# Performance work log

Measured on AMD Instinct MI355X. Metric: run time of the kernel, lower is better.

The kernel has to match this reference:

```python
import jax, jax.numpy as jnp
import numpy as np

EPS = 1e-8
TEMP = 0.1

def setup_inputs() -> dict:
    key = jax.random.key(0)
    k1, k2, k3, k4, k5 = jax.random.split(key, 5)
    B, C, S, D = 4096, 1000, 5, 2048
    return {
        "query": jax.random.normal(k1, (B, D), dtype=jnp.float32),
        "labels": jax.random.randint(k2, (B,), 0, C),
        "memory_keys": jax.random.normal(k3, (C, S, D), dtype=jnp.float32),
        "memory_values": jax.random.normal(k4, (C, S, D), dtype=jnp.float32),
        "quality_scores": jax.random.uniform(k5, (C, S), dtype=jnp.float32),
        "top_k": 3,
    }

def reference(query, labels, memory_keys, memory_values, quality_scores, top_k):
    # Gather per-sample class slices: (B, S, D) and (B, S)
    class_keys = memory_keys[labels]
    class_vals = memory_values[labels]
    class_scores = quality_scores[labels]

    # Cosine similarity between query[i] and its class's slot keys
    qn = query / jnp.maximum(jnp.linalg.norm(query, axis=-1, keepdims=True), EPS)
    kn = class_keys / jnp.maximum(jnp.linalg.norm(class_keys, axis=-1, keepdims=True), EPS)
    sim = jnp.einsum('bd,bsd->bs', qn, kn)           # (B, S)
    combined = sim * class_scores                    # (B, S)

    k = min(int(top_k), class_scores.shape[1])
    top_scores, top_idx = jax.lax.top_k(combined, k) # (B, k)
    attn = jax.nn.softmax(top_scores / TEMP, axis=-1)
    top_vals = jnp.take_along_axis(class_vals, top_idx[..., None], axis=1)  # (B, k, D)
    retrieved = jnp.einsum('bk,bkd->bd', attn, top_vals)                    # (B, D)

    # miss handling: classes whose quality scores sum to 0 yield zeros
    hit = class_scores.sum(axis=1) != 0              # (B,)
    retrieved = jnp.where(hit[:, None], retrieved, 0.0)
    weights = jnp.where(hit, top_scores.mean(axis=-1), 0.0)
    return retrieved, weights
```

## Files before the change

### kernel.cpp

```cpp
#include <hip/hip_runtime.h>
#include <math.h>

#define NSLOT 5
#define EPSF 1e-8f
#define WPB 4

typedef float f4 __attribute__((ext_vector_type(4)));


__global__ void hist_kernel(const int* __restrict__ labels, int* __restrict__ counts, int B) {
    int i = blockIdx.x * blockDim.x + threadIdx.x;
    if (i < B) atomicAdd(&counts[labels[i]], 1);
}

__global__ void scan_kernel(const int* __restrict__ counts, int* __restrict__ cursor, int C) {
    __shared__ int sh[1024];
    __shared__ int running;
    if (threadIdx.x == 0) running = 0;
    __syncthreads();
    for (int base = 0; base < C; base += 1024) {
        int t = base + threadIdx.x;
        int v = (t < C) ? counts[t] : 0;
        sh[threadIdx.x] = v;
        __syncthreads();
        for (int d = 1; d < 1024; d <<= 1) {
            int x = (threadIdx.x >= d) ? sh[threadIdx.x - d] : 0;
            __syncthreads();
            sh[threadIdx.x] += x;
            __syncthreads();
        }
        int excl = sh[threadIdx.x] - v + running;
        if (t < C) cursor[t] = excl;
        __syncthreads();
        if (threadIdx.x == 0) running += sh[1023];
        __syncthreads();
    }
}

__global__ void scatter_kernel(const int* __restrict__ labels, int* __restrict__ cursor,
                               int* __restrict__ bucket, int B) {
    int i = blockIdx.x * blockDim.x + threadIdx.x;
    if (i < B) {
        int slot = atomicAdd(&cursor[labels[i]], 1);
        bucket[slot] = i;
    }
}


template<int N4T>
__global__ __launch_bounds__(64 * WPB, 4) void mb_wave_kernel(
    const float* __restrict__ query,
    const float* __restrict__ mkeys,
    const float* __restrict__ mvals,
    const float* __restrict__ qscores,
    const int*   __restrict__ topk_p,
    const int*   __restrict__ labels,
    const int*   __restrict__ bucket,
    float* __restrict__ out_ret,
    float* __restrict__ out_w,
    int B, int n4_rt)
{
    const int tid  = threadIdx.x;
    const int lane = tid & 63;
    const int wave = tid >> 6;

    int j;
    if (bucket) {
        const int stripe = B >> 3;
        j = (blockIdx.x & 7) * stripe + (blockIdx.x >> 3) * WPB + wave;
    } else {
        j = blockIdx.x * WPB + wave;
    }
    if (j >= B) return;
    const int i = bucket ? bucket[j] : j;
    const int c = labels[i];

    int k = topk_p[0];
    if (k > NSLOT) k = NSLOT;
    if (k < 1) k = 1;

    const int n4 = (N4T > 0) ? N4T : n4_rt;
    const f4* q4 = reinterpret_cast<const f4*>(query) + (size_t)i * n4;
    const f4* k4 = reinterpret_cast<const f4*>(mkeys) + (size_t)c * NSLOT * n4;
    const f4* v4 = reinterpret_cast<const f4*>(mvals) + (size_t)c * NSLOT * n4;
    f4*       o4 = reinterpret_cast<f4*>(out_ret) + (size_t)i * n4;

    float qq = 0.f;
    float dot[NSLOT], kk[NSLOT];
#pragma unroll
    for (int s = 0; s < NSLOT; ++s) { dot[s] = 0.f; kk[s] = 0.f; }

    for (int idx = lane; idx < n4; idx += 64) {
        f4 q = q4[idx];
        qq = fmaf(q.x, q.x, fmaf(q.y, q.y, fmaf(q.z, q.z, fmaf(q.w, q.w, qq))));
#pragma unroll
        for (int s = 0; s < NSLOT; ++s) {
            f4 kv = k4[s * n4 + idx];
            dot[s] = fmaf(q.x, kv.x, fmaf(q.y, kv.y, fmaf(q.z, kv.z, fmaf(q.w, kv.w, dot[s]))));
            kk[s]  = fmaf(kv.x, kv.x, fmaf(kv.y, kv.y, fmaf(kv.z, kv.z, fmaf(kv.w, kv.w, kk[s]))));
        }
    }

#pragma unroll
    for (int off = 1; off < 64; off <<= 1) {
        qq += __shfl_xor(qq, off);
#pragma unroll
        for (int s = 0; s < NSLOT; ++s) {
            dot[s] += __shfl_xor(dot[s], off);
            kk[s]  += __shfl_xor(kk[s], off);
        }
    }

    float qn = fmaxf(sqrtf(qq), EPSF);

    float scr[NSLOT];
    float ssum = 0.f;
#pragma unroll
    for (int s = 0; s < NSLOT; ++s) {
        scr[s] = qscores[(size_t)c * NSLOT + s];
        ssum += scr[s];
    }

    float comb[NSLOT];
#pragma unroll
    for (int s = 0; s < NSLOT; ++s) {
        float kn = fmaxf(sqrtf(kk[s]), EPSF);
        comb[s] = (dot[s] / (qn * kn)) * scr[s];
    }

    bool used[NSLOT];
#pragma unroll
    for (int s = 0; s < NSLOT; ++s) used[s] = false;
    float tsc[NSLOT];
    int   tix[NSLOT];
#pragma unroll
    for (int jj = 0; jj < NSLOT; ++jj) {
        float best = -INFINITY;
        int bi = 0;
        if (jj < k) {
#pragma unroll
            for (int s = 0; s < NSLOT; ++s) {
                if (!used[s] && comb[s] > best) { best = comb[s]; bi = s; }
            }
#pragma unroll
            for (int s = 0; s < NSLOT; ++s) used[s] = used[s] || (s == bi);
        }
        tsc[jj] = best;
        tix[jj] = bi;
    }

    const bool hit = (ssum != 0.0f);
    float m = tsc[0];
    float esum = 0.f, wsum = 0.f;
    float a[NSLOT];
#pragma unroll
    for (int jj = 0; jj < NSLOT; ++jj) {
        if (jj < k) {
            a[jj] = __expf((tsc[jj] - m) * 10.0f);
            esum += a[jj];
            wsum += tsc[jj];
        } else {
            a[jj] = 0.f;
        }
    }
    float inv = hit ? (1.0f / esum) : 0.0f;

    float wgt[NSLOT];
#pragma unroll
    for (int s = 0; s < NSLOT; ++s) {
        float ws = 0.f;
#pragma unroll
        for (int jj = 0; jj < NSLOT; ++jj)
            if (jj < k && tix[jj] == s) ws += a[jj] * inv;
        wgt[s] = ws;
    }

    if (lane == 0) out_w[i] = hit ? (wsum / (float)k) : 0.0f;

    for (int idx = lane; idx < n4; idx += 64) {
        f4 acc = (f4)(0.f);
#pragma unroll
        for (int s = 0; s < NSLOT; ++s) {
            f4 v = v4[s * n4 + idx];
            acc.x = fmaf(wgt[s], v.x, acc.x);
            acc.y = fmaf(wgt[s], v.y, acc.y);
            acc.z = fmaf(wgt[s], v.z, acc.z);
            acc.w = fmaf(wgt[s], v.w, acc.w);
        }
        o4[idx] = acc;
    }
}

extern "C" void kernel_launch(void* const* d_in, const int* in_sizes, int n_in,
                              void* d_out, int out_size, void* d_ws, size_t ws_size,
                              hipStream_t stream) {
    const float* query   = (const float*)d_in[0];
    const int*   labels  = (const int*)d_in[1];
    const float* mkeys   = (const float*)d_in[2];
    const float* mvals   = (const float*)d_in[3];
    const float* qscores = (const float*)d_in[4];
    const int*   topk    = (const int*)d_in[5];

    const int B  = in_sizes[1];
    const int D  = in_sizes[0] / B;
    const int n4 = D >> 2;
    const int C  = in_sizes[4] / NSLOT;

    float* out_ret = (float*)d_out;
    float* out_w   = out_ret + (size_t)B * D;

    const bool can_bin = (B % 32 == 0) &&
                         ((size_t)(2 * C + B) * sizeof(int) <= ws_size);

    const int* bucket = nullptr;
    if (can_bin) {
        int* counts = (int*)d_ws;
        int* bkt    = counts + 2 * C;
        hipMemsetAsync(counts, 0, (size_t)C * sizeof(int), stream);
        hist_kernel<<<dim3((B + 255) / 256), dim3(256), 0, stream>>>(labels, counts, B);
        scan_kernel<<<dim3(1), dim3(1024), 0, stream>>>(counts, counts + C, C);
        scatter_kernel<<<dim3((B + 255) / 256), dim3(256), 0, stream>>>(labels, counts + C, bkt, B);
        bucket = bkt;
    }

    dim3 grid((B + WPB - 1) / WPB), block(64 * WPB);
    if (D == 2048) {
        mb_wave_kernel<512><<<grid, block, 0, stream>>>(
            query, mkeys, mvals, qscores, topk, labels, bucket, out_ret, out_w, B, n4);
    } else if (D == 1024) {
        mb_wave_kernel<256><<<grid, block, 0, stream>>>(
            query, mkeys, mvals, qscores, topk, labels, bucket, out_ret, out_w, B, n4);
    } else {
        mb_wave_kernel<0><<<grid, block, 0, stream>>>(
            query, mkeys, mvals, qscores, topk, labels, bucket, out_ret, out_w, B, n4);
    }
}
```

Measured before the change: 40.42 us.

## Split each sample across two waves and gather only top-k value slots

Result: no change. 40.60 us (+0.5%).

```diff
diff --git a/kernel.cpp b/kernel.cpp
--- a/kernel.cpp
+++ b/kernel.cpp
@@ -3,7 +3,6 @@
 
 #define NSLOT 5
 #define EPSF 1e-8f
-#define WPB 4
 
 typedef float f4 __attribute__((ext_vector_type(4)));
 
@@ -47,8 +46,7 @@
 }
 
 
-template<int N4T>
-__global__ __launch_bounds__(64 * WPB, 4) void mb_wave_kernel(
+__global__ __launch_bounds__(256, 8) void mb_main_kernel(
     const float* __restrict__ query,
     const float* __restrict__ mkeys,
     const float* __restrict__ mvals,
@@ -58,28 +56,29 @@
     const int*   __restrict__ bucket,
     float* __restrict__ out_ret,
     float* __restrict__ out_w,
-    int B, int n4_rt)
+    int B)
 {
     const int tid  = threadIdx.x;
     const int lane = tid & 63;
     const int wave = tid >> 6;
+    const int ws   = wave & 1;
+    const int sidx = wave >> 1;
 
     int j;
     if (bucket) {
-        const int stripe = B >> 3;
-        j = (blockIdx.x & 7) * stripe + (blockIdx.x >> 3) * WPB + wave;
+        j = (blockIdx.x & 7) * (B >> 3) + (blockIdx.x >> 3) * 2 + sidx;
     } else {
-        j = blockIdx.x * WPB + wave;
-    }
-    if (j >= B) return;
-    const int i = bucket ? bucket[j] : j;
-    const int c = labels[i];
+        j = blockIdx.x * 2 + sidx;
+    }
+    const bool active = (j < B);
+    const int i = active ? (bucket ? bucket[j] : j) : 0;
+    const int c = active ? labels[i] : 0;
 
     int k = topk_p[0];
     if (k > NSLOT) k = NSLOT;
     if (k < 1) k = 1;
 
-    const int n4 = (N4T > 0) ? N4T : n4_rt;
+    const int n4 = 512;
     const f4* q4 = reinterpret_cast<const f4*>(query) + (size_t)i * n4;
     const f4* k4 = reinterpret_cast<const f4*>(mkeys) + (size_t)c * NSLOT * n4;
     const f4* v4 = reinterpret_cast<const f4*>(mvals) + (size_t)c * NSLOT * n4;
@@ -90,14 +89,18 @@
 #pragma unroll
     for (int s = 0; s < NSLOT; ++s) { dot[s] = 0.f; kk[s] = 0.f; }
 
-    for (int idx = lane; idx < n4; idx += 64) {
-        f4 q = q4[idx];
-        qq = fmaf(q.x, q.x, fmaf(q.y, q.y, fmaf(q.z, q.z, fmaf(q.w, q.w, qq))));
-#pragma unroll
-        for (int s = 0; s < NSLOT; ++s) {
-            f4 kv = k4[s * n4 + idx];
-            dot[s] = fmaf(q.x, kv.x, fmaf(q.y, kv.y, fmaf(q.z, kv.z, fmaf(q.w, kv.w, dot[s]))));
-            kk[s]  = fmaf(kv.x, kv.x, fmaf(kv.y, kv.y, fmaf(kv.z, kv.z, fmaf(kv.w, kv.w, kk[s]))));
+    if (active) {
+#pragma unroll
+        for (int m = 0; m < 4; ++m) {
+            const int idx = lane + (ws * 4 + m) * 64;
+            f4 q = q4[idx];
+            qq = fmaf(q.x, q.x, fmaf(q.y, q.y, fmaf(q.z, q.z, fmaf(q.w, q.w, qq))));
+#pragma unroll
+            for (int s = 0; s < NSLOT; ++s) {
+                f4 kv = k4[s * n4 + idx];
+                dot[s] = fmaf(q.x, kv.x, fmaf(q.y, kv.y, fmaf(q.z, kv.z, fmaf(q.w, kv.w, dot[s]))));
+                kk[s]  = fmaf(kv.x, kv.x, fmaf(kv.y, kv.y, fmaf(kv.z, kv.z, fmaf(kv.w, kv.w, kk[s]))));
+            }
         }
     }
 
@@ -110,6 +113,25 @@
             kk[s]  += __shfl_xor(kk[s], off);
         }
     }
+
+    __shared__ float red[2][2][11];
+    if (lane == 0) {
+        red[sidx][ws][0] = qq;
+#pragma unroll
+        for (int s = 0; s < NSLOT; ++s) {
+            red[sidx][ws][1 + s] = dot[s];
+            red[sidx][ws][6 + s] = kk[s];
+        }
+    }
+    __syncthreads();
+    qq = red[sidx][0][0] + red[sidx][1][0];
+#pragma unroll
+    for (int s = 0; s < NSLOT; ++s) {
+        dot[s] = red[sidx][0][1 + s] + red[sidx][1][1 + s];
+        kk[s]  = red[sidx][0][6 + s] + red[sidx][1][6 + s];
+    }
+
+    if (!active) return;
 
     float qn = fmaxf(sqrtf(qq), EPSF);
 
@@ -165,27 +187,131 @@
     }
     float inv = hit ? (1.0f / esum) : 0.0f;
 
-    float wgt[NSLOT];
-#pragma unroll
+    if (ws == 0 && lane == 0) out_w[i] = hit ? (wsum / (float)k) : 0.0f;
+
+    if (k == 3) {
+        const float a0 = a[0] * inv, a1 = a[1] * inv, a2 = a[2] * inv;
+        const f4* p0 = v4 + tix[0] * n4;
+        const f4* p1 = v4 + tix[1] * n4;
+        const f4* p2 = v4 + tix[2] * n4;
+#pragma unroll
+        for (int m2 = 0; m2 < 4; ++m2) {
+            const int idx = lane + (ws * 4 + m2) * 64;
+            f4 v0 = p0[idx];
+            f4 v1 = p1[idx];
+            f4 v2 = p2[idx];
+            f4 acc;
+            acc.x = fmaf(a0, v0.x, fmaf(a1, v1.x, a2 * v2.x));
+            acc.y = fmaf(a0, v0.y, fmaf(a1, v1.y, a2 * v2.y));
+            acc.z = fmaf(a0, v0.z, fmaf(a1, v1.z, a2 * v2.z));
+            acc.w = fmaf(a0, v0.w, fmaf(a1, v1.w, a2 * v2.w));
+            o4[idx] = acc;
+        }
+    } else {
+        float wgt[NSLOT];
+#pragma unroll
+        for (int s = 0; s < NSLOT; ++s) {
+            float wsv = 0.f;
+#pragma unroll
+            for (int jj = 0; jj < NSLOT; ++jj)
+                if (jj < k && tix[jj] == s) wsv += a[jj] * inv;
+            wgt[s] = wsv;
+        }
+#pragma unroll
+        for (int m2 = 0; m2 < 4; ++m2) {
+            const int idx = lane + (ws * 4 + m2) * 64;
+            f4 acc = (f4)(0.f);
+#pragma unroll
+            for (int s = 0; s < NSLOT; ++s) {
+                f4 v = v4[s * n4 + idx];
+                acc.x = fmaf(wgt[s], v.x, acc.x);
+                acc.y = fmaf(wgt[s], v.y, acc.y);
+                acc.z = fmaf(wgt[s], v.z, acc.z);
+                acc.w = fmaf(wgt[s], v.w, acc.w);
+            }
+            o4[idx] = acc;
+        }
+    }
+}
+
+
+__global__ __launch_bounds__(64) void mb_generic_kernel(
+    const float* __restrict__ query,
+    const int*   __restrict__ labels,
+    const float* __restrict__ mkeys,
+    const float* __restrict__ mvals,
+    const float* __restrict__ qscores,
+    const int*   __restrict__ topk_p,
+    float* __restrict__ out_ret,
+    float* __restrict__ out_w,
+    int B, int n4)
+{
+    const int lane = threadIdx.x;
+    const int i    = blockIdx.x;
+    if (i >= B) return;
+    const int c = labels[i];
+    int k = topk_p[0];
+    if (k > NSLOT) k = NSLOT;
+    if (k < 1) k = 1;
+
+    const f4* q4 = reinterpret_cast<const f4*>(query) + (size_t)i * n4;
+    const f4* k4 = reinterpret_cast<const f4*>(mkeys) + (size_t)c * NSLOT * n4;
+    const f4* v4 = reinterpret_cast<const f4*>(mvals) + (size_t)c * NSLOT * n4;
+    f4*       o4 = reinterpret_cast<f4*>(out_ret) + (size_t)i * n4;
+
+    float qq = 0.f, dot[NSLOT] = {0}, kk[NSLOT] = {0};
+    for (int idx = lane; idx < n4; idx += 64) {
+        f4 q = q4[idx];
+        qq = fmaf(q.x, q.x, fmaf(q.y, q.y, fmaf(q.z, q.z, fmaf(q.w, q.w, qq))));
+        for (int s = 0; s < NSLOT; ++s) {
+            f4 t = k4[s * n4 + idx];
+            dot[s] = fmaf(q.x, t.x, fmaf(q.y, t.y, fmaf(q.z, t.z, fmaf(q.w, t.w, dot[s]))));
+            kk[s]  = fmaf(t.x, t.x, fmaf(t.y, t.y, fmaf(t.z, t.z, fmaf(t.w, t.w, kk[s]))));
+        }
+    }
+    for (int o = 1; o < 64; o <<= 1) {
+        qq += __shfl_xor(qq, o);
+        for (int s = 0; s < NSLOT; ++s) {
+            dot[s] += __shfl_xor(dot[s], o);
+            kk[s]  += __shfl_xor(kk[s], o);
+        }
+    }
+    float qn = fmaxf(sqrtf(qq), EPSF);
+    float scr[NSLOT], ssum = 0.f;
+    for (int s = 0; s < NSLOT; ++s) { scr[s] = qscores[(size_t)c * NSLOT + s]; ssum += scr[s]; }
+    float comb[NSLOT];
+    for (int s = 0; s < NSLOT; ++s)
+        comb[s] = (dot[s] / (qn * fmaxf(sqrtf(kk[s]), EPSF))) * scr[s];
+    bool used[NSLOT] = {false, false, false, false, false};
+    float tsc[NSLOT]; int tix[NSLOT];
+    for (int jj = 0; jj < NSLOT; ++jj) {
+        float best = -INFINITY; int bi = 0;
+        if (jj < k) {
+            for (int s = 0; s < NSLOT; ++s)
+                if (!used[s] && comb[s] > best) { best = comb[s]; bi = s; }
+            used[bi] = true;
+        }
+        tsc[jj] = best; tix[jj] = bi;
+    }
+    const bool hit = (ssum != 0.0f);
+    float m = tsc[0], esum = 0.f, wsum = 0.f, a[NSLOT];
+    for (int jj = 0; jj < NSLOT; ++jj) {
+        if (jj < k) { a[jj] = __expf((tsc[jj] - m) * 10.0f); esum += a[jj]; wsum += tsc[jj]; }
+        else a[jj] = 0.f;
+    }
+    float inv = hit ? (1.0f / esum) : 0.0f;
+    float w[NSLOT];
     for (int s = 0; s < NSLOT; ++s) {
-        float ws = 0.f;
-#pragma unroll
-        for (int jj = 0; jj < NSLOT; ++jj)
-            if (jj < k && tix[jj] == s) ws += a[jj] * inv;
-        wgt[s] = ws;
-    }
-
+        float wsv = 0.f;
+        for (int jj = 0; jj < NSLOT; ++jj) if (jj < k && tix[jj] == s) wsv += a[jj] * inv;
+        w[s] = wsv;
+    }
     if (lane == 0) out_w[i] = hit ? (wsum / (float)k) : 0.0f;
-
     for (int idx = lane; idx < n4; idx += 64) {
         f4 acc = (f4)(0.f);
-#pragma unroll
         for (int s = 0; s < NSLOT; ++s) {
             f4 v = v4[s * n4 + idx];
-            acc.x = fmaf(wgt[s], v.x, acc.x);
-            acc.y = fmaf(wgt[s], v.y, acc.y);
-            acc.z = fmaf(wgt[s], v.z, acc.z);
-            acc.w = fmaf(wgt[s], v.w, acc.w);
+            acc += v * w[s];
         }
         o4[idx] = acc;
     }
@@ -209,29 +335,23 @@
     float* out_ret = (float*)d_out;
     float* out_w   = out_ret + (size_t)B * D;
 
-    const bool can_bin = (B % 32 == 0) &&
-                         ((size_t)(2 * C + B) * sizeof(int) <= ws_size);
-
-    const int* bucket = nullptr;
-    if (can_bin) {
+    if (D == 2048 && (B % 16 == 0) &&
+        ((size_t)(2 * C + B) * sizeof(int) <= ws_size)) {
         int* counts = (int*)d_ws;
+        int* cursor = counts + C;
         int* bkt    = counts + 2 * C;
         hipMemsetAsync(counts, 0, (size_t)C * sizeof(int), stream);
         hist_kernel<<<dim3((B + 255) / 256), dim3(256), 0, stream>>>(labels, counts, B);
-        scan_kernel<<<dim3(1), dim3(1024), 0, stream>>>(counts, counts + C, C);
-        scatter_kernel<<<dim3((B + 255) / 256), dim3(256), 0, stream>>>(labels, counts + C, bkt, B);
-        bucket = bkt;
-    }
-
-    dim3 grid((B + WPB - 1) / WPB), block(64 * WPB);
-    if (D == 2048) {
-        mb_wave_kernel<512><<<grid, block, 0, stream>>>(
-            query, mkeys, mvals, qscores, topk, labels, bucket, out_ret, out_w, B, n4);
-    } else if (D == 1024) {
-        mb_wave_kernel<256><<<grid, block, 0, stream>>>(
-            query, mkeys, mvals, qscores, topk, labels, bucket, out_ret, out_w, B, n4);
+        scan_kernel<<<dim3(1), dim3(1024), 0, stream>>>(counts, cursor, C);
+        scatter_kernel<<<dim3((B + 255) / 256), dim3(256), 0, stream>>>(labels, cursor, bkt, B);
+
+        mb_main_kernel<<<dim3(B / 2), dim3(256), 0, stream>>>(
+            query, mkeys, mvals, qscores, topk, labels, bkt, out_ret, out_w, B);
+    } else if (D == 2048) {
+        mb_main_kernel<<<dim3((B + 1) / 2), dim3(256), 0, stream>>>(
+            query, mkeys, mvals, qscores, topk, labels, nullptr, out_ret, out_w, B);
     } else {
-        mb_wave_kernel<0><<<grid, block, 0, stream>>>(
-            query, mkeys, mvals, qscores, topk, labels, bucket, out_ret, out_w, B, n4);
-    }
-}
+        mb_generic_kernel<<<dim3(B), dim3(64), 0, stream>>>(
+            query, labels, mkeys, mvals, qscores, topk, out_ret, out_w, B, n4);
+    }
+}
```
